# Kernel optimization log

Measured on AMD Instinct MI355X. Metric: run time of the kernel, lower is better.

## Reference

```python
import jax, jax.numpy as jnp
import numpy as np

N = 32768        # atoms
INV = 256        # irreps_in[inv_field].dim (scalar latent width)
MUL = 32         # input eq multiplicity: '32x1o'
VOUT = 4         # output eq multiplicity: '4x1o'
HID = 512        # ScalarMLPFunction latent dims [512, 512]
INV_OUT = 2      # inv_out_irreps '2x0e'
TYPES = 32       # num_types
EPS = 1e-10


def _mlp(x, w1, w2, w3):
    # ScalarMLPFunction: Linear(+1/sqrt(fan_in) norm) -> SiLU -> ... -> Linear
    h = jax.nn.silu((x @ w1) * (1.0 / np.sqrt(w1.shape[0])))
    h = jax.nn.silu((h @ w2) * (1.0 / np.sqrt(w2.shape[0])))
    return (h @ w3) * (1.0 / np.sqrt(w3.shape[0]))


def setup_inputs() -> dict:
    key = jax.random.key(0)
    ks = jax.random.split(key, 10)
    inv_features = jax.random.normal(ks[0], (N, INV), dtype=jnp.float32)
    eq_features = jax.random.normal(ks[1], (N, MUL, 3), dtype=jnp.float32)
    atom_types = jax.random.randint(ks[2], (N, 1), 0, TYPES, dtype=jnp.int32)
    # hypernetwork (final_latent): INV -> 512 -> 512 -> MUL*VOUT
    w1_lat = jax.random.normal(ks[3], (INV, HID), dtype=jnp.float32)
    w2_lat = jax.random.normal(ks[4], (HID, HID), dtype=jnp.float32)
    w3_lat = jax.random.normal(ks[5], (HID, MUL * VOUT), dtype=jnp.float32)
    # final_readout: INV -> 512 -> 512 -> INV_OUT
    w1_ro = jax.random.normal(ks[6], (INV, HID), dtype=jnp.float32)
    w2_ro = jax.random.normal(ks[7], (HID, HID), dtype=jnp.float32)
    w3_ro = jax.random.normal(ks[8], (HID, INV_OUT), dtype=jnp.float32)
    # atom_type2bond_lengths parameter, init to ones as in the module
    bond_lengths = jnp.ones((TYPES, VOUT, 1), dtype=jnp.float32)
    return dict(inv_features=inv_features, eq_features=eq_features,
                atom_types=atom_types, w1_lat=w1_lat, w2_lat=w2_lat,
                w3_lat=w3_lat, w1_ro=w1_ro, w2_ro=w2_ro, w3_ro=w3_ro,
                bond_lengths=bond_lengths)


def reference(inv_features, eq_features, atom_types, w1_lat, w2_lat, w3_lat,
              w1_ro, w2_ro, w3_ro, bond_lengths):
    # hypernet-generated per-atom weights for the equivariant Linear
    weights = _mlp(inv_features, w1_lat, w2_lat, w3_lat)          # [N, MUL*VOUT]
    weights = weights.reshape(-1, MUL, VOUT)                      # [N, u, v]
    inv_out = _mlp(inv_features, w1_ro, w2_ro, w3_ro)             # [N, INV_OUT]
    # e3nn Linear '32x1o -> 4x1o', shared_weights=False, path norm 1/sqrt(mul_in)
    eq = jnp.einsum('num,nuv->nvm', eq_features, weights) * (1.0 / np.sqrt(MUL))
    # norm -> divide -> nan_to_num
    norm = jnp.linalg.norm(eq, axis=-1, keepdims=True)            # [N, VOUT, 1]
    eq = jnp.nan_to_num(eq / (norm + EPS), nan=0.0)
    # per-atom-type bond-length scale (gather-multiply)
    eq = eq * bond_lengths[atom_types[:, 0]]                      # [N, VOUT, 3]
    return inv_out, eq
```

## Files before the change

kernel.cpp:

```cpp
#include <hip/hip_runtime.h>
#include <hip/hip_bf16.h>

#define N_ATOMS 32768

typedef __attribute__((ext_vector_type(4))) float f32x4;
typedef __attribute__((ext_vector_type(8))) short bf16x8;
typedef unsigned short u16;

__device__ __forceinline__ u16 f2b(float f) {
    union { __hip_bfloat16 b; u16 u; } c;
    c.b = __float2bfloat16(f);
    return c.u;
}
__device__ __forceinline__ float b2f(u16 u) {
    union { unsigned int i; float f; } c;
    c.i = ((unsigned int)u) << 16;
    return c.f;
}

#define GLDS16(src, dst) __builtin_amdgcn_global_load_lds( \
    (const __attribute__((address_space(1))) void*)(src),  \
    (__attribute__((address_space(3))) void*)(dst), 16, 0, 0)


__global__ void convx_kernel(const float* __restrict__ x,
                             u16* __restrict__ xhi, u16* __restrict__ xlo) {
    size_t i = (size_t)(blockIdx.x * 256 + threadIdx.x) * 8;
    float4 v0 = *(const float4*)(x + i);
    float4 v1 = *(const float4*)(x + i + 4);
    float v[8] = {v0.x, v0.y, v0.z, v0.w, v1.x, v1.y, v1.z, v1.w};
    bf16x8 rh, rl;
#pragma unroll
    for (int j = 0; j < 8; ++j) {
        u16 h = f2b(v[j]);
        rh[j] = (short)h;
        rl[j] = (short)f2b(v[j] - b2f(h));
    }
    *(bf16x8*)(xhi + i) = rh;
    *(bf16x8*)(xlo + i) = rl;
}

__global__ void convw_kernel(const float* __restrict__ w1l, const float* __restrict__ w2l,
                             const float* __restrict__ w3l, const float* __restrict__ w1r,
                             const float* __restrict__ w2r,
                             u16* __restrict__ W1LThi, u16* __restrict__ W1LTlo,
                             u16* __restrict__ W1RT,
                             u16* __restrict__ W2LThi, u16* __restrict__ W2LTlo,
                             u16* __restrict__ W2RT,
                             u16* __restrict__ W3LThi, u16* __restrict__ W3LTlo) {
    int i = blockIdx.x * 256 + threadIdx.x;
    if (i < 131072) {
        int n = i >> 8, k = i & 255;
        float v = w1l[k * 512 + n];
        u16 h = f2b(v);
        W1LThi[i] = h;
        W1LTlo[i] = f2b(v - b2f(h));
    } else if (i < 262144) {
        int j = i - 131072;
        int n = j >> 8, k = j & 255;
        W1RT[j] = f2b(w1r[k * 512 + n]);
    } else if (i < 524288) {
        int j = i - 262144;
        int n = j >> 9, k = j & 511;
        float v = w2l[k * 512 + n];
        u16 h = f2b(v);
        W2LThi[j] = h;
        W2LTlo[j] = f2b(v - b2f(h));
    } else if (i < 786432) {
        int j = i - 524288;
        int n = j >> 9, k = j & 511;
        W2RT[j] = f2b(w2r[k * 512 + n]);
    } else if (i < 851968) {
        int j = i - 786432;
        int n = j >> 9, k = j & 511;
        float v = w3l[k * 128 + n];
        u16 h = f2b(v);
        W3LThi[j] = h;
        W3LTlo[j] = f2b(v - b2f(h));
    }
}

template<int NSEG, int GX, bool SILU, int OUTK>
__global__ void __launch_bounds__(256, 2) gemm_multi(
        const u16* __restrict__ Ahi, const u16* __restrict__ Alo,
        const u16* __restrict__ Bhi, const u16* __restrict__ Blo,
        void* __restrict__ Chi, void* __restrict__ Clo,
        int ldc, int K, float scale) {
    __shared__ __align__(16) u16 lA[2][128 * 64];
    __shared__ __align__(16) u16 lB[2][128 * 64];
    const int tid = threadIdx.x;
    const int lane = tid & 63;
    const int wid = tid >> 6;
    const int wr = wid >> 1, wc = wid & 1;
    const int rlane = lane & 15;
    const int kc = lane >> 4;

    const int nwg = gridDim.x;
    const int bid = blockIdx.x;
    const int wg = (bid & 7) * (nwg >> 3) + (bid >> 3);
    const int bn = (wg % GX) * 128;
    const int bm = (wg / GX) * 128;

    const int kt = K >> 6;
    const int NT = NSEG * kt;

    auto stage = [&](int t, int buf) {
        int seg = (NSEG == 1) ? 0 : ((t >= kt) + (t >= 2 * kt));
        const u16* As = (NSEG == 1) ? Ahi : (seg == 1 ? Alo : Ahi);
        const u16* Bs = (NSEG == 1) ? Bhi : (seg == 2 ? Blo : Bhi);
        int k0 = (t - seg * kt) << 6;
        u16* la = lA[buf];
        u16* lb = lB[buf];
#pragma unroll
        for (int call = 0; call < 4; ++call) {
            int id = call * 256 + tid;
            int row = id >> 3, cp = id & 7;
            int c = cp ^ (row & 7);
            GLDS16(As + (size_t)(bm + row) * K + k0 + c * 8, la + id * 8);
            GLDS16(Bs + (size_t)(bn + row) * K + k0 + c * 8, lb + id * 8);
        }
    };

    f32x4 acc[4][4] = {};

    auto compute = [&](int buf) {
        const u16* la = lA[buf];
        const u16* lb = lB[buf];
        bf16x8 af[2][4], bfr[2][4];
#pragma unroll
        for (int ks = 0; ks < 2; ++ks) {
#pragma unroll
            for (int m = 0; m < 4; ++m) {
                int row = wr * 64 + m * 16 + rlane;
                int cp = (ks * 4 + kc) ^ (row & 7);
                af[ks][m] = *(const bf16x8*)&la[row * 64 + cp * 8];
            }
#pragma unroll
            for (int n = 0; n < 4; ++n) {
                int row = wc * 64 + n * 16 + rlane;
                int cp = (ks * 4 + kc) ^ (row & 7);
                bfr[ks][n] = *(const bf16x8*)&lb[row * 64 + cp * 8];
            }
        }
#pragma unroll
        for (int m = 0; m < 4; ++m)
#pragma unroll
            for (int n = 0; n < 4; ++n) {
                acc[m][n] = __builtin_amdgcn_mfma_f32_16x16x32_bf16(af[0][m], bfr[0][n], acc[m][n], 0, 0, 0);
                acc[m][n] = __builtin_amdgcn_mfma_f32_16x16x32_bf16(af[1][m], bfr[1][n], acc[m][n], 0, 0, 0);
            }
    };

    stage(0, 0);
    for (int t = 0; t < NT - 1; ++t) {
        __builtin_amdgcn_s_barrier();
        stage(t + 1, (t + 1) & 1);
        __builtin_amdgcn_sched_barrier(0);
        asm volatile("s_waitcnt vmcnt(8)" ::: "memory");
        __builtin_amdgcn_s_barrier();
        __builtin_amdgcn_sched_barrier(0);
        compute(t & 1);
    }
    asm volatile("s_waitcnt vmcnt(0)" ::: "memory");
    __builtin_amdgcn_s_barrier();
    __builtin_amdgcn_sched_barrier(0);
    compute((NT - 1) & 1);

#pragma unroll
    for (int m = 0; m < 4; ++m) {
        int grow0 = bm + wr * 64 + m * 16 + ((lane >> 4) << 2);
#pragma unroll
        for (int n = 0; n < 4; ++n) {
            int gcol = bn + wc * 64 + n * 16 + rlane;
#pragma unroll
            for (int r = 0; r < 4; ++r) {
                float v = acc[m][n][r] * scale;
                if constexpr (SILU) v = v / (1.0f + __expf(-v));
                size_t idx = (size_t)(grow0 + r) * ldc + gcol;
                if constexpr (OUTK == 0) {
                    ((float*)Chi)[idx] = v;
                } else if constexpr (OUTK == 1) {
                    ((u16*)Chi)[idx] = f2b(v);
                } else {
                    u16 h = f2b(v);
                    ((u16*)Chi)[idx] = h;
                    ((u16*)Clo)[idx] = f2b(v - b2f(h));
                }
            }
        }
    }
}

__global__ void invout_kernel(const u16* __restrict__ H2b,
                              const float* __restrict__ w3,
                              float* __restrict__ out) {
    int g = blockIdx.x * 256 + threadIdx.x;
    int n = g >> 6;
    int lane = g & 63;
    bf16x8 hv = *(const bf16x8*)(H2b + (size_t)n * 512 + lane * 8);
    float s0 = 0.f, s1 = 0.f;
#pragma unroll
    for (int j = 0; j < 8; ++j) {
        float hf = b2f((u16)hv[j]);
        int k = lane * 8 + j;
        s0 = fmaf(hf, w3[2 * k], s0);
        s1 = fmaf(hf, w3[2 * k + 1], s1);
    }
#pragma unroll
    for (int off = 32; off > 0; off >>= 1) {
        s0 += __shfl_xor(s0, off);
        s1 += __shfl_xor(s1, off);
    }
    if (lane == 0) {
        const float s = 0.04419417382415922f;
        out[2 * n] = s0 * s;
        out[2 * n + 1] = s1 * s;
    }
}

__global__ void eq_kernel(const float* __restrict__ eqf, const float* __restrict__ wgt,
                          const int* __restrict__ types, const float* __restrict__ bond,
                          float* __restrict__ out) {
    int t = blockIdx.x * 256 + threadIdx.x;
    int n = t >> 2, v = t & 3;
    const float* e = eqf + (size_t)n * 96;
    const float* w = wgt + (size_t)n * 128 + v;
    float a0 = 0.f, a1 = 0.f, a2 = 0.f;
#pragma unroll
    for (int u = 0; u < 32; ++u) {
        float wv = w[u * 4];
        a0 = fmaf(e[u * 3 + 0], wv, a0);
        a1 = fmaf(e[u * 3 + 1], wv, a1);
        a2 = fmaf(e[u * 3 + 2], wv, a2);
    }
    const float s = 0.17677669529663687f;
    a0 *= s; a1 *= s; a2 *= s;
    float norm = sqrtf(a0 * a0 + a1 * a1 + a2 * a2) + 1e-10f;
    float bl = bond[types[n] * 4 + v];
    float r0 = a0 / norm, r1 = a1 / norm, r2 = a2 / norm;
    if (isnan(r0)) r0 = 0.f;
    if (isnan(r1)) r1 = 0.f;
    if (isnan(r2)) r2 = 0.f;
    out[(size_t)n * 12 + v * 3 + 0] = r0 * bl;
    out[(size_t)n * 12 + v * 3 + 1] = r1 * bl;
    out[(size_t)n * 12 + v * 3 + 2] = r2 * bl;
}

extern "C" void kernel_launch(void* const* d_in, const int* in_sizes, int n_in,
                              void* d_out, int out_size, void* d_ws, size_t ws_size,
                              hipStream_t stream) {
    const float* inv  = (const float*)d_in[0];
    const float* eqf  = (const float*)d_in[1];
    const int*   typs = (const int*)d_in[2];
    const float* w1l  = (const float*)d_in[3];
    const float* w2l  = (const float*)d_in[4];
    const float* w3l  = (const float*)d_in[5];
    const float* w1r  = (const float*)d_in[6];
    const float* w2r  = (const float*)d_in[7];
    const float* w3r  = (const float*)d_in[8];
    const float* bond = (const float*)d_in[9];

    char* ws = (char*)d_ws;
    const size_t MB = 1024 * 1024, KB = 1024;
    u16* XHI   = (u16*)(ws);
    u16* XLO   = (u16*)(ws + 16 * MB);
    u16* H1R   = (u16*)(ws + 32 * MB);
    u16* H1Lhi = (u16*)(ws + 64 * MB);
    u16* H1Llo = (u16*)(ws + 96 * MB);
    u16* H2R   = (u16*)(ws + 128 * MB);
    u16* H2Lhi = (u16*)(ws);
    u16* H2Llo = (u16*)(ws + 32 * MB);
    float* WGT = (float*)(ws + 64 * MB);
    char* wb = ws + 160 * MB;
    u16* W1LThi = (u16*)(wb);
    u16* W1LTlo = (u16*)(wb + 256 * KB);
    u16* W1RT   = (u16*)(wb + 512 * KB);
    u16* W2LThi = (u16*)(wb + 768 * KB);
    u16* W2LTlo = (u16*)(wb + 1280 * KB);
    u16* W2RT   = (u16*)(wb + 1792 * KB);
    u16* W3LThi = (u16*)(wb + 2304 * KB);
    u16* W3LTlo = (u16*)(wb + 2432 * KB);

    float* out_inv = (float*)d_out;
    float* out_eq  = (float*)d_out + N_ATOMS * 2;

    const float s256 = 0.0625f;
    const float s512 = 0.04419417382415922f;

    convx_kernel<<<dim3(4096), dim3(256), 0, stream>>>(inv, XHI, XLO);
    convw_kernel<<<dim3(3328), dim3(256), 0, stream>>>(w1l, w2l, w3l, w1r, w2r,
        W1LThi, W1LTlo, W1RT, W2LThi, W2LTlo, W2RT, W3LThi, W3LTlo);

    gemm_multi<3, 4, true, 2><<<dim3(1024), dim3(256), 0, stream>>>(
        XHI, XLO, W1LThi, W1LTlo, H1Lhi, H1Llo, 512, 256, s256);
    gemm_multi<1, 4, true, 1><<<dim3(1024), dim3(256), 0, stream>>>(
        XHI, nullptr, W1RT, nullptr, H1R, nullptr, 512, 256, s256);
    gemm_multi<1, 4, true, 1><<<dim3(1024), dim3(256), 0, stream>>>(
        H1R, nullptr, W2RT, nullptr, H2R, nullptr, 512, 512, s512);
    gemm_multi<3, 4, true, 2><<<dim3(1024), dim3(256), 0, stream>>>(
        H1Lhi, H1Llo, W2LThi, W2LTlo, H2Lhi, H2Llo, 512, 512, s512);
    gemm_multi<3, 1, false, 0><<<dim3(256), dim3(256), 0, stream>>>(
        H2Lhi, H2Llo, W3LThi, W3LTlo, WGT, nullptr, 128, 512, s512);
    invout_kernel<<<dim3(8192), dim3(256), 0, stream>>>(H2R, w3r, out_inv);
    eq_kernel<<<dim3(512), dim3(256), 0, stream>>>(eqf, WGT, typs, bond, out_eq);
}
```

Measured before the change: 216.4 us.

## Add 256x256-tile 8-wave GEMM kernel for the hidden-layer MLP GEMMs

Adds a new GEMM kernel with 256x256 output tiles, 512 threads (8 waves, each computing 128x64), swizzled LDS staging and prefetch interleaved between the two k-substeps. The four hidden-layer GEMMs switch to it with 256 workgroups instead of 1024 128x128 tiles, aiming for more operand reuse per LDS load and less global traffic. The cost is 128KB of LDS per block and 128 accumulator registers per lane, which lowers occupancy. With only 256 blocks on a 256-CU part, there may be a single wave of blocks and poor latency hiding.

```diff
diff --git a/kernel.cpp b/kernel.cpp
--- a/kernel.cpp
+++ b/kernel.cpp
@@ -81,6 +81,129 @@
 }
 
 template<int NSEG, int GX, bool SILU, int OUTK>
+__global__ void __launch_bounds__(512, 2) gemm8p(
+        const u16* __restrict__ Ahi, const u16* __restrict__ Alo,
+        const u16* __restrict__ Bhi, const u16* __restrict__ Blo,
+        void* __restrict__ Chi, void* __restrict__ Clo,
+        int ldc, int K, float scale) {
+    __shared__ __align__(16) u16 lA[2][256 * 64];
+    __shared__ __align__(16) u16 lB[2][256 * 64];
+    const int tid = threadIdx.x;
+    const int lane = tid & 63;
+    const int wid = tid >> 6;
+    const int wm = wid >> 2;
+    const int wn = wid & 3;
+    const int rlane = lane & 15;
+    const int kc = lane >> 4;
+    const int cps = rlane & 7;
+
+    const int nwg = gridDim.x;
+    const int bid = blockIdx.x;
+    const int wg = (bid & 7) * (nwg >> 3) + (bid >> 3);
+    const int bn = (wg % GX) * 256;
+    const int bm = (wg / GX) * 256;
+
+    const int kt = K >> 6;
+    const int NT = NSEG * kt;
+
+    const int srow = tid >> 3;
+    const int scp = tid & 7;
+
+    auto stageA = [&](int t, int buf) {
+        int seg = (NSEG == 1) ? 0 : ((t >= kt) + (t >= 2 * kt));
+        const u16* As = (NSEG == 1) ? Ahi : (seg == 1 ? Alo : Ahi);
+        int k0 = (t - seg * kt) << 6;
+        u16* la = lA[buf];
+#pragma unroll
+        for (int call = 0; call < 4; ++call) {
+            int row = call * 64 + srow;
+            int c = scp ^ (row & 7);
+            GLDS16(As + (size_t)(bm + row) * K + k0 + c * 8, la + (size_t)(row * 64 + scp * 8));
+        }
+    };
+    auto stageB = [&](int t, int buf) {
+        int seg = (NSEG == 1) ? 0 : ((t >= kt) + (t >= 2 * kt));
+        const u16* Bs = (NSEG == 1) ? Bhi : (seg == 2 ? Blo : Bhi);
+        int k0 = (t - seg * kt) << 6;
+        u16* lb = lB[buf];
+#pragma unroll
+        for (int call = 0; call < 4; ++call) {
+            int row = call * 64 + srow;
+            int c = scp ^ (row & 7);
+            GLDS16(Bs + (size_t)(bn + row) * K + k0 + c * 8, lb + (size_t)(row * 64 + scp * 8));
+        }
+    };
+
+    f32x4 acc[8][4] = {};
+
+    stageA(0, 0);
+    stageB(0, 0);
+    asm volatile("s_waitcnt vmcnt(0)" ::: "memory");
+    __builtin_amdgcn_s_barrier();
+
+    for (int t = 0; t < NT; ++t) {
+        const int cur = t & 1, nxt = cur ^ 1;
+        const bool pf = (t + 1 < NT);
+        const u16* la = lA[cur];
+        const u16* lb = lB[cur];
+#pragma unroll
+        for (int ks = 0; ks < 2; ++ks) {
+            bf16x8 af[8], bfr[4];
+            const int cp = (ks * 4 + kc) ^ cps;
+#pragma unroll
+            for (int m = 0; m < 8; ++m) {
+                int row = wm * 128 + m * 16 + rlane;
+                af[m] = *(const bf16x8*)&la[row * 64 + cp * 8];
+            }
+#pragma unroll
+            for (int n = 0; n < 4; ++n) {
+                int row = wn * 64 + n * 16 + rlane;
+                bfr[n] = *(const bf16x8*)&lb[row * 64 + cp * 8];
+            }
+            if (pf) {
+                if (ks == 0) stageA(t + 1, nxt);
+                else         stageB(t + 1, nxt);
+            }
+            asm volatile("s_waitcnt lgkmcnt(0)" ::: "memory");
+            __builtin_amdgcn_sched_barrier(0);
+            __builtin_amdgcn_s_setprio(1);
+#pragma unroll
+            for (int m = 0; m < 8; ++m)
+#pragma unroll
+                for (int n = 0; n < 4; ++n)
+                    acc[m][n] = __builtin_amdgcn_mfma_f32_16x16x32_bf16(af[m], bfr[n], acc[m][n], 0, 0, 0);
+            __builtin_amdgcn_s_setprio(0);
+        }
+        asm volatile("s_waitcnt vmcnt(0)" ::: "memory");
+        __builtin_amdgcn_s_barrier();
+    }
+
+#pragma unroll
+    for (int m = 0; m < 8; ++m) {
+        int grow0 = bm + wm * 128 + m * 16 + ((lane >> 4) << 2);
+#pragma unroll
+        for (int n = 0; n < 4; ++n) {
+            int gcol = bn + wn * 64 + n * 16 + rlane;
+#pragma unroll
+            for (int r = 0; r < 4; ++r) {
+                float v = acc[m][n][r] * scale;
+                if constexpr (SILU) v = v / (1.0f + __expf(-v));
+                size_t idx = (size_t)(grow0 + r) * ldc + gcol;
+                if constexpr (OUTK == 0) {
+                    ((float*)Chi)[idx] = v;
+                } else if constexpr (OUTK == 1) {
+                    ((u16*)Chi)[idx] = f2b(v);
+                } else {
+                    u16 h = f2b(v);
+                    ((u16*)Chi)[idx] = h;
+                    ((u16*)Clo)[idx] = f2b(v - b2f(h));
+                }
+            }
+        }
+    }
+}
+
+template<int NSEG, int GX, bool SILU, int OUTK>
 __global__ void __launch_bounds__(256, 2) gemm_multi(
         const u16* __restrict__ Ahi, const u16* __restrict__ Alo,
         const u16* __restrict__ Bhi, const u16* __restrict__ Blo,
@@ -291,13 +414,13 @@
     convw_kernel<<<dim3(3328), dim3(256), 0, stream>>>(w1l, w2l, w3l, w1r, w2r,
         W1LThi, W1LTlo, W1RT, W2LThi, W2LTlo, W2RT, W3LThi, W3LTlo);
 
-    gemm_multi<3, 4, true, 2><<<dim3(1024), dim3(256), 0, stream>>>(
+    gemm8p<3, 2, true, 2><<<dim3(256), dim3(512), 0, stream>>>(
         XHI, XLO, W1LThi, W1LTlo, H1Lhi, H1Llo, 512, 256, s256);
-    gemm_multi<1, 4, true, 1><<<dim3(1024), dim3(256), 0, stream>>>(
+    gemm8p<1, 2, true, 1><<<dim3(256), dim3(512), 0, stream>>>(
         XHI, nullptr, W1RT, nullptr, H1R, nullptr, 512, 256, s256);
-    gemm_multi<1, 4, true, 1><<<dim3(1024), dim3(256), 0, stream>>>(
+    gemm8p<1, 2, true, 1><<<dim3(256), dim3(512), 0, stream>>>(
         H1R, nullptr, W2RT, nullptr, H2R, nullptr, 512, 512, s512);
-    gemm_multi<3, 4, true, 2><<<dim3(1024), dim3(256), 0, stream>>>(
+    gemm8p<3, 2, true, 2><<<dim3(256), dim3(512), 0, stream>>>(
         H1Lhi, H1Llo, W2LThi, W2LTlo, H2Lhi, H2Llo, 512, 512, s512);
     gemm_multi<3, 1, false, 0><<<dim3(256), dim3(256), 0, stream>>>(
         H2Lhi, H2Llo, W3LThi, W3LTlo, WGT, nullptr, 128, 512, s512);
```

Measured after the change: 205.0 us. -5.3%, faster.

## Enlarge GEMM tiles to 256x256 with 8 waves and interleaved prefetch/MFMA schedule

Applied to the files above, without the earlier changes.

Replaces the 128x128, 4-wave GEMM with a 256xNF*64 tile run by 512 threads (2x4 waves). Each wave computes a 128x64 subtile. Global-to-LDS prefetch of the next K tile is split into chunks and interleaved with four LDS-read/MFMA phases, with s_setprio raised around the MFMAs. The larger tiles are meant to raise arithmetic intensity and overlap loads with compute. In exchange, grids shrink to 256 or 128 blocks, which may leave CUs underfilled on a 256-CU part, and register pressure rises.

```diff
diff --git a/kernel.cpp b/kernel.cpp
--- a/kernel.cpp
+++ b/kernel.cpp
@@ -80,98 +80,129 @@
     }
 }
 
-template<int NSEG, int GX, bool SILU, int OUTK>
-__global__ void __launch_bounds__(256, 2) gemm_multi(
+template<int NSEG, int GX, int NF, bool SILU, int OUTK>
+__global__ void __launch_bounds__(512, 2) gemm_p4(
         const u16* __restrict__ Ahi, const u16* __restrict__ Alo,
         const u16* __restrict__ Bhi, const u16* __restrict__ Blo,
         void* __restrict__ Chi, void* __restrict__ Clo,
         int ldc, int K, float scale) {
-    __shared__ __align__(16) u16 lA[2][128 * 64];
-    __shared__ __align__(16) u16 lB[2][128 * 64];
+    __shared__ __align__(16) u16 lA[2][256 * 64];
+    __shared__ __align__(16) u16 lB[2][NF * 64 * 64];
     const int tid = threadIdx.x;
     const int lane = tid & 63;
     const int wid = tid >> 6;
-    const int wr = wid >> 1, wc = wid & 1;
+    const int wm = wid >> 2;
+    const int wn = wid & 3;
     const int rlane = lane & 15;
     const int kc = lane >> 4;
+    const int cps = rlane & 7;
+    const int srow = tid >> 3;
+    const int scp = tid & 7;
 
     const int nwg = gridDim.x;
     const int bid = blockIdx.x;
     const int wg = (bid & 7) * (nwg >> 3) + (bid >> 3);
-    const int bn = (wg % GX) * 128;
-    const int bm = (wg / GX) * 128;
+    const int bn = (wg % GX) * (NF * 64);
+    const int bm = (wg / GX) * 256;
 
     const int kt = K >> 6;
     const int NT = NSEG * kt;
 
-    auto stage = [&](int t, int buf) {
-        int seg = (NSEG == 1) ? 0 : ((t >= kt) + (t >= 2 * kt));
-        const u16* As = (NSEG == 1) ? Ahi : (seg == 1 ? Alo : Ahi);
-        const u16* Bs = (NSEG == 1) ? Bhi : (seg == 2 ? Blo : Bhi);
-        int k0 = (t - seg * kt) << 6;
-        u16* la = lA[buf];
-        u16* lb = lB[buf];
-#pragma unroll
-        for (int call = 0; call < 4; ++call) {
-            int id = call * 256 + tid;
-            int row = id >> 3, cp = id & 7;
-            int c = cp ^ (row & 7);
-            GLDS16(As + (size_t)(bm + row) * K + k0 + c * 8, la + id * 8);
-            GLDS16(Bs + (size_t)(bn + row) * K + k0 + c * 8, lb + id * 8);
-        }
-    };
-
-    f32x4 acc[4][4] = {};
-
-    auto compute = [&](int buf) {
-        const u16* la = lA[buf];
-        const u16* lb = lB[buf];
-        bf16x8 af[2][4], bfr[2][4];
-#pragma unroll
-        for (int ks = 0; ks < 2; ++ks) {
-#pragma unroll
-            for (int m = 0; m < 4; ++m) {
-                int row = wr * 64 + m * 16 + rlane;
-                int cp = (ks * 4 + kc) ^ (row & 7);
-                af[ks][m] = *(const bf16x8*)&la[row * 64 + cp * 8];
-            }
-#pragma unroll
-            for (int n = 0; n < 4; ++n) {
-                int row = wc * 64 + n * 16 + rlane;
-                int cp = (ks * 4 + kc) ^ (row & 7);
-                bfr[ks][n] = *(const bf16x8*)&lb[row * 64 + cp * 8];
-            }
-        }
-#pragma unroll
-        for (int m = 0; m < 4; ++m)
-#pragma unroll
-            for (int n = 0; n < 4; ++n) {
-                acc[m][n] = __builtin_amdgcn_mfma_f32_16x16x32_bf16(af[0][m], bfr[0][n], acc[m][n], 0, 0, 0);
-                acc[m][n] = __builtin_amdgcn_mfma_f32_16x16x32_bf16(af[1][m], bfr[1][n], acc[m][n], 0, 0, 0);
-            }
-    };
-
-    stage(0, 0);
-    for (int t = 0; t < NT - 1; ++t) {
-        __builtin_amdgcn_s_barrier();
-        stage(t + 1, (t + 1) & 1);
-        __builtin_amdgcn_sched_barrier(0);
-        asm volatile("s_waitcnt vmcnt(8)" ::: "memory");
-        __builtin_amdgcn_s_barrier();
-        __builtin_amdgcn_sched_barrier(0);
-        compute(t & 1);
-    }
-    asm volatile("s_waitcnt vmcnt(0)" ::: "memory");
-    __builtin_amdgcn_s_barrier();
-    __builtin_amdgcn_sched_barrier(0);
-    compute((NT - 1) & 1);
-
-#pragma unroll
-    for (int m = 0; m < 4; ++m) {
-        int grow0 = bm + wr * 64 + m * 16 + ((lane >> 4) << 2);
-#pragma unroll
-        for (int n = 0; n < 4; ++n) {
-            int gcol = bn + wc * 64 + n * 16 + rlane;
+#define STA(tt, bb, c) do {                                                   \
+        int seg_ = (NSEG == 1) ? 0 : (((tt) >= kt) + ((tt) >= 2 * kt));       \
+        const u16* As_ = (NSEG == 1) ? Ahi : (seg_ == 1 ? Alo : Ahi);         \
+        int k0_ = ((tt) - seg_ * kt) << 6;                                    \
+        int row_ = (c) * 64 + srow;                                           \
+        GLDS16(As_ + (size_t)(bm + row_) * K + k0_ + (scp ^ (srow & 7)) * 8,  \
+               &lA[bb][row_ * 64 + scp * 8]);                                 \
+    } while (0)
+#define STB(tt, bb, c) do {                                                   \
+        int seg_ = (NSEG == 1) ? 0 : (((tt) >= kt) + ((tt) >= 2 * kt));       \
+        const u16* Bs_ = (NSEG == 1) ? Bhi : (seg_ == 2 ? Blo : Bhi);         \
+        int k0_ = ((tt) - seg_ * kt) << 6;                                    \
+        int row_ = (c) * 64 + srow;                                           \
+        GLDS16(Bs_ + (size_t)(bn + row_) * K + k0_ + (scp ^ (srow & 7)) * 8,  \
+               &lB[bb][row_ * 64 + scp * 8]);                                 \
+    } while (0)
+#define READ_AF(dst, bb, mh, ks) do {                                         \
+        _Pragma("unroll")                                                     \
+        for (int m_ = 0; m_ < 4; ++m_) {                                      \
+            int row_ = wm * 128 + (mh) * 64 + m_ * 16 + rlane;                \
+            dst[m_] = *(const bf16x8*)&lA[bb][row_ * 64 + (((ks) * 4 + kc) ^ cps) * 8]; \
+        }                                                                     \
+    } while (0)
+#define READ_BF(dst, bb, ks) do {                                             \
+        _Pragma("unroll")                                                     \
+        for (int n_ = 0; n_ < NF; ++n_) {                                     \
+            int row_ = wn * (NF * 16) + n_ * 16 + rlane;                      \
+            dst[n_] = *(const bf16x8*)&lB[bb][row_ * 64 + (((ks) * 4 + kc) ^ cps) * 8]; \
+        }                                                                     \
+    } while (0)
+#define MFMA4(af_, bf_, mh) do {                                              \
+        __builtin_amdgcn_s_setprio(1);                                        \
+        _Pragma("unroll")                                                     \
+        for (int m_ = 0; m_ < 4; ++m_)                                        \
+            _Pragma("unroll")                                                 \
+            for (int n_ = 0; n_ < NF; ++n_)                                   \
+                acc[(mh) * 4 + m_][n_] = __builtin_amdgcn_mfma_f32_16x16x32_bf16( \
+                    af_[m_], bf_[n_], acc[(mh) * 4 + m_][n_], 0, 0, 0);       \
+        __builtin_amdgcn_s_setprio(0);                                        \
+    } while (0)
+#define LGKM0 do {                                                            \
+        asm volatile("s_waitcnt lgkmcnt(0)" ::: "memory");                    \
+        __builtin_amdgcn_sched_barrier(0);                                    \
+    } while (0)
+
+#define TILE(tt, cur, PF) do {                                                \
+        __builtin_amdgcn_s_barrier();                                         \
+        bf16x8 bfA[NF], bfB[NF], af0[4], af1[4], af2[4], af3[4];              \
+                                                          \
+        if (PF) { STB(tt + 1, (cur) ^ 1, 0); STB(tt + 1, (cur) ^ 1, 1);       \
+                  asm volatile("s_waitcnt vmcnt(4)" ::: "memory"); }          \
+        else    { asm volatile("s_waitcnt vmcnt(0)" ::: "memory"); }          \
+        READ_BF(bfA, cur, 0); READ_AF(af0, cur, 0, 0);                        \
+        LGKM0; MFMA4(af0, bfA, 0);                                            \
+                                                          \
+        if (PF) { if (NF == 4) { STB(tt + 1, (cur) ^ 1, 2); STB(tt + 1, (cur) ^ 1, 3); } \
+                  else         { STA(tt + 1, (cur) ^ 1, 0); STA(tt + 1, (cur) ^ 1, 2); } \
+                  asm volatile("s_waitcnt vmcnt(4)" ::: "memory"); }          \
+        READ_AF(af1, cur, 1, 0);                                              \
+        LGKM0; MFMA4(af1, bfA, 1);                                            \
+                                                          \
+        if (PF) { if (NF == 4) { STA(tt + 1, (cur) ^ 1, 0); STA(tt + 1, (cur) ^ 1, 2); } \
+                  else         { STA(tt + 1, (cur) ^ 1, 1); STA(tt + 1, (cur) ^ 1, 3); } } \
+        READ_BF(bfB, cur, 1); READ_AF(af2, cur, 0, 1);                        \
+        LGKM0; MFMA4(af2, bfB, 0);                                            \
+                                                          \
+        if (PF) { if (NF == 4) { STA(tt + 1, (cur) ^ 1, 1); STA(tt + 1, (cur) ^ 1, 3); } } \
+        READ_AF(af3, cur, 1, 1);                                              \
+        LGKM0; MFMA4(af3, bfB, 1);                                            \
+    } while (0)
+
+    f32x4 acc[8][NF] = {};
+
+    STB(0, 0, 0); STB(0, 0, 1);
+    if (NF == 4) { STB(0, 0, 2); STB(0, 0, 3); }
+    STA(0, 0, 0); STA(0, 0, 2); STA(0, 0, 1); STA(0, 0, 3);
+
+    for (int t = 0; t < NT - 1; ++t)
+        TILE(t, t & 1, true);
+    TILE(NT - 1, (NT - 1) & 1, false);
+
+#undef TILE
+#undef LGKM0
+#undef MFMA4
+#undef READ_BF
+#undef READ_AF
+#undef STB
+#undef STA
+
+#pragma unroll
+    for (int m = 0; m < 8; ++m) {
+        int grow0 = bm + wm * 128 + m * 16 + ((lane >> 4) << 2);
+#pragma unroll
+        for (int n = 0; n < NF; ++n) {
+            int gcol = bn + wn * (NF * 16) + n * 16 + rlane;
 #pragma unroll
             for (int r = 0; r < 4; ++r) {
                 float v = acc[m][n][r] * scale;
@@ -291,15 +322,15 @@
     convw_kernel<<<dim3(3328), dim3(256), 0, stream>>>(w1l, w2l, w3l, w1r, w2r,
         W1LThi, W1LTlo, W1RT, W2LThi, W2LTlo, W2RT, W3LThi, W3LTlo);
 
-    gemm_multi<3, 4, true, 2><<<dim3(1024), dim3(256), 0, stream>>>(
+    gemm_p4<3, 2, 4, true, 2><<<dim3(256), dim3(512), 0, stream>>>(
         XHI, XLO, W1LThi, W1LTlo, H1Lhi, H1Llo, 512, 256, s256);
-    gemm_multi<1, 4, true, 1><<<dim3(1024), dim3(256), 0, stream>>>(
+    gemm_p4<1, 2, 4, true, 1><<<dim3(256), dim3(512), 0, stream>>>(
         XHI, nullptr, W1RT, nullptr, H1R, nullptr, 512, 256, s256);
-    gemm_multi<1, 4, true, 1><<<dim3(1024), dim3(256), 0, stream>>>(
+    gemm_p4<1, 2, 4, true, 1><<<dim3(256), dim3(512), 0, stream>>>(
         H1R, nullptr, W2RT, nullptr, H2R, nullptr, 512, 512, s512);
-    gemm_multi<3, 4, true, 2><<<dim3(1024), dim3(256), 0, stream>>>(
+    gemm_p4<3, 2, 4, true, 2><<<dim3(256), dim3(512), 0, stream>>>(
         H1Lhi, H1Llo, W2LThi, W2LTlo, H2Lhi, H2Llo, 512, 512, s512);
-    gemm_multi<3, 1, false, 0><<<dim3(256), dim3(256), 0, stream>>>(
+    gemm_p4<3, 1, 2, false, 0><<<dim3(128), dim3(512), 0, stream>>>(
         H2Lhi, H2Llo, W3LThi, W3LTlo, WGT, nullptr, 128, 512, s512);
     invout_kernel<<<dim3(8192), dim3(256), 0, stream>>>(H2R, w3r, out_inv);
     eq_kernel<<<dim3(512), dim3(256), 0, stream>>>(eqf, WGT, typs, bond, out_eq);
```

Measured after the change: 236.3 us. 9.2% more time.

## Rework GEMM into 256-row tiles with 512 threads and triple-buffered K=32 pipeline

Applied to the files above, without the earlier changes.

Replaces the 128x128 double-buffered GEMM with a kernel using 256xNF*64 tiles, 8 waves per block, K-step of 32 and a three-stage LDS ring that prefetches two steps ahead. Each wave computes a 128xNF*16 sub-tile, which gives more MFMA work per LDS fragment load. The loop uses a single barrier per step and raises wave priority around the MFMA block. The aim is better data reuse and latency hiding. The trade-off is fewer workgroups (256 or 128), which may underfill the CUs, plus higher register pressure from the 8xNF accumulators.

```diff
diff --git a/kernel.cpp b/kernel.cpp
--- a/kernel.cpp
+++ b/kernel.cpp
@@ -80,98 +80,104 @@
     }
 }
 
-template<int NSEG, int GX, bool SILU, int OUTK>
-__global__ void __launch_bounds__(256, 2) gemm_multi(
+template<int NSEG, int GX, int NF, bool SILU, int OUTK>
+__global__ void __launch_bounds__(512, 2) gemm_r3(
         const u16* __restrict__ Ahi, const u16* __restrict__ Alo,
         const u16* __restrict__ Bhi, const u16* __restrict__ Blo,
         void* __restrict__ Chi, void* __restrict__ Clo,
         int ldc, int K, float scale) {
-    __shared__ __align__(16) u16 lA[2][128 * 64];
-    __shared__ __align__(16) u16 lB[2][128 * 64];
+    __shared__ __align__(16) u16 lA[3][256 * 32];
+    __shared__ __align__(16) u16 lB[3][NF * 64 * 32];
+    constexpr int LPT = 2 + NF / 2;
     const int tid = threadIdx.x;
     const int lane = tid & 63;
     const int wid = tid >> 6;
-    const int wr = wid >> 1, wc = wid & 1;
+    const int wm = wid >> 2;
+    const int wn = wid & 3;
     const int rlane = lane & 15;
     const int kc = lane >> 4;
+    const int chp = (kc ^ ((rlane >> 1) & 3)) * 8;
+    const int srow = tid >> 2;
+    const int scp = tid & 3;
+    const int cs = scp ^ ((srow >> 1) & 3);
 
     const int nwg = gridDim.x;
     const int bid = blockIdx.x;
     const int wg = (bid & 7) * (nwg >> 3) + (bid >> 3);
-    const int bn = (wg % GX) * 128;
-    const int bm = (wg / GX) * 128;
-
-    const int kt = K >> 6;
+    const int bn = (wg % GX) * (NF * 64);
+    const int bm = (wg / GX) * 256;
+
+    const int kt = K >> 5;
     const int NT = NSEG * kt;
 
-    auto stage = [&](int t, int buf) {
+    auto stage = [&](int t, int b) {
         int seg = (NSEG == 1) ? 0 : ((t >= kt) + (t >= 2 * kt));
         const u16* As = (NSEG == 1) ? Ahi : (seg == 1 ? Alo : Ahi);
         const u16* Bs = (NSEG == 1) ? Bhi : (seg == 2 ? Blo : Bhi);
-        int k0 = (t - seg * kt) << 6;
-        u16* la = lA[buf];
-        u16* lb = lB[buf];
-#pragma unroll
-        for (int call = 0; call < 4; ++call) {
-            int id = call * 256 + tid;
-            int row = id >> 3, cp = id & 7;
-            int c = cp ^ (row & 7);
-            GLDS16(As + (size_t)(bm + row) * K + k0 + c * 8, la + id * 8);
-            GLDS16(Bs + (size_t)(bn + row) * K + k0 + c * 8, lb + id * 8);
+        int k0 = (t - seg * kt) << 5;
+        u16* la = lA[b];
+        u16* lb = lB[b];
+#pragma unroll
+        for (int c = 0; c < 2; ++c) {
+            int row = c * 128 + srow;
+            GLDS16(As + (size_t)(bm + row) * K + k0 + cs * 8, la + row * 32 + scp * 8);
+        }
+#pragma unroll
+        for (int c = 0; c < NF / 2; ++c) {
+            int row = c * 128 + srow;
+            GLDS16(Bs + (size_t)(bn + row) * K + k0 + cs * 8, lb + row * 32 + scp * 8);
         }
     };
 
-    f32x4 acc[4][4] = {};
-
-    auto compute = [&](int buf) {
-        const u16* la = lA[buf];
-        const u16* lb = lB[buf];
-        bf16x8 af[2][4], bfr[2][4];
-#pragma unroll
-        for (int ks = 0; ks < 2; ++ks) {
-#pragma unroll
-            for (int m = 0; m < 4; ++m) {
-                int row = wr * 64 + m * 16 + rlane;
-                int cp = (ks * 4 + kc) ^ (row & 7);
-                af[ks][m] = *(const bf16x8*)&la[row * 64 + cp * 8];
-            }
-#pragma unroll
-            for (int n = 0; n < 4; ++n) {
-                int row = wc * 64 + n * 16 + rlane;
-                int cp = (ks * 4 + kc) ^ (row & 7);
-                bfr[ks][n] = *(const bf16x8*)&lb[row * 64 + cp * 8];
-            }
-        }
-#pragma unroll
-        for (int m = 0; m < 4; ++m)
-#pragma unroll
-            for (int n = 0; n < 4; ++n) {
-                acc[m][n] = __builtin_amdgcn_mfma_f32_16x16x32_bf16(af[0][m], bfr[0][n], acc[m][n], 0, 0, 0);
-                acc[m][n] = __builtin_amdgcn_mfma_f32_16x16x32_bf16(af[1][m], bfr[1][n], acc[m][n], 0, 0, 0);
-            }
-    };
+    f32x4 acc[8][NF] = {};
 
     stage(0, 0);
-    for (int t = 0; t < NT - 1; ++t) {
+    stage(1, 1);
+    if constexpr (LPT == 4) asm volatile("s_waitcnt vmcnt(4)" ::: "memory");
+    else                    asm volatile("s_waitcnt vmcnt(3)" ::: "memory");
+    __builtin_amdgcn_s_barrier();
+
+    int cur = 0;
+    for (int t = 0; t < NT; ++t) {
+        if (t + 2 < NT) stage(t + 2, cur == 0 ? 2 : cur - 1);
+        const u16* la = lA[cur];
+        const u16* lb = lB[cur];
+        bf16x8 af[8], bf[NF];
+#pragma unroll
+        for (int m = 0; m < 8; ++m) {
+            int row = wm * 128 + m * 16 + rlane;
+            af[m] = *(const bf16x8*)&la[row * 32 + chp];
+        }
+#pragma unroll
+        for (int n = 0; n < NF; ++n) {
+            int row = wn * (NF * 16) + n * 16 + rlane;
+            bf[n] = *(const bf16x8*)&lb[row * 32 + chp];
+        }
+        asm volatile("s_waitcnt lgkmcnt(0)" ::: "memory");
+        __builtin_amdgcn_sched_barrier(0);
+        __builtin_amdgcn_s_setprio(1);
+#pragma unroll
+        for (int m = 0; m < 8; ++m)
+#pragma unroll
+            for (int n = 0; n < NF; ++n)
+                acc[m][n] = __builtin_amdgcn_mfma_f32_16x16x32_bf16(af[m], bf[n], acc[m][n], 0, 0, 0);
+        __builtin_amdgcn_s_setprio(0);
+        if (t + 2 < NT) {
+            if constexpr (LPT == 4) asm volatile("s_waitcnt vmcnt(4)" ::: "memory");
+            else                    asm volatile("s_waitcnt vmcnt(3)" ::: "memory");
+        } else {
+            asm volatile("s_waitcnt vmcnt(0)" ::: "memory");
+        }
         __builtin_amdgcn_s_barrier();
-        stage(t + 1, (t + 1) & 1);
-        __builtin_amdgcn_sched_barrier(0);
-        asm volatile("s_waitcnt vmcnt(8)" ::: "memory");
-        __builtin_amdgcn_s_barrier();
-        __builtin_amdgcn_sched_barrier(0);
-        compute(t & 1);
-    }
-    asm volatile("s_waitcnt vmcnt(0)" ::: "memory");
-    __builtin_amdgcn_s_barrier();
-    __builtin_amdgcn_sched_barrier(0);
-    compute((NT - 1) & 1);
-
-#pragma unroll
-    for (int m = 0; m < 4; ++m) {
-        int grow0 = bm + wr * 64 + m * 16 + ((lane >> 4) << 2);
-#pragma unroll
-        for (int n = 0; n < 4; ++n) {
-            int gcol = bn + wc * 64 + n * 16 + rlane;
+        cur = (cur == 2) ? 0 : cur + 1;
+    }
+
+#pragma unroll
+    for (int m = 0; m < 8; ++m) {
+        int grow0 = bm + wm * 128 + m * 16 + ((lane >> 4) << 2);
+#pragma unroll
+        for (int n = 0; n < NF; ++n) {
+            int gcol = bn + wn * (NF * 16) + n * 16 + rlane;
 #pragma unroll
             for (int r = 0; r < 4; ++r) {
                 float v = acc[m][n][r] * scale;
@@ -291,15 +297,15 @@
     convw_kernel<<<dim3(3328), dim3(256), 0, stream>>>(w1l, w2l, w3l, w1r, w2r,
         W1LThi, W1LTlo, W1RT, W2LThi, W2LTlo, W2RT, W3LThi, W3LTlo);
 
-    gemm_multi<3, 4, true, 2><<<dim3(1024), dim3(256), 0, stream>>>(
+    gemm_r3<3, 2, 4, true, 2><<<dim3(256), dim3(512), 0, stream>>>(
         XHI, XLO, W1LThi, W1LTlo, H1Lhi, H1Llo, 512, 256, s256);
-    gemm_multi<1, 4, true, 1><<<dim3(1024), dim3(256), 0, stream>>>(
+    gemm_r3<1, 2, 4, true, 1><<<dim3(256), dim3(512), 0, stream>>>(
         XHI, nullptr, W1RT, nullptr, H1R, nullptr, 512, 256, s256);
-    gemm_multi<1, 4, true, 1><<<dim3(1024), dim3(256), 0, stream>>>(
+    gemm_r3<1, 2, 4, true, 1><<<dim3(256), dim3(512), 0, stream>>>(
         H1R, nullptr, W2RT, nullptr, H2R, nullptr, 512, 512, s512);
-    gemm_multi<3, 4, true, 2><<<dim3(1024), dim3(256), 0, stream>>>(
+    gemm_r3<3, 2, 4, true, 2><<<dim3(256), dim3(512), 0, stream>>>(
         H1Lhi, H1Llo, W2LThi, W2LTlo, H2Lhi, H2Llo, 512, 512, s512);
-    gemm_multi<3, 1, false, 0><<<dim3(256), dim3(256), 0, stream>>>(
+    gemm_r3<3, 1, 2, false, 0><<<dim3(128), dim3(512), 0, stream>>>(
         H2Lhi, H2Llo, W3LThi, W3LTlo, WGT, nullptr, 128, 512, s512);
     invout_kernel<<<dim3(8192), dim3(256), 0, stream>>>(H2R, w3r, out_inv);
     eq_kernel<<<dim3(512), dim3(256), 0, stream>>>(eqf, WGT, typs, bond, out_eq);
```

Measured after the change: 251.5 us. 1.16x slower.
